# Performance work log

Hardware: AMD Instinct MI355X
Metric: run time of the kernel (lower is better)

## Reference

```python
import jax, jax.numpy as jnp
import numpy as np

N_NODES = 10000
N_EDGES = 160000
D_IN = 50
ALPHA = 0.2  # LeakyReLU negative slope


def _xavier(key, shape):
    fan_in, fan_out = shape[0], int(np.prod(shape[1:]))
    limit = float(np.sqrt(6.0 / (fan_in + fan_out)))
    return jax.random.uniform(key, shape, jnp.float32, -limit, limit)


def setup_inputs() -> dict:
    key = jax.random.key(0)
    ks = jax.random.split(key, 8)
    x = jax.random.normal(ks[0], (N_NODES, D_IN), jnp.float32)
    edge_idx = jax.random.randint(ks[1], (2, N_EDGES), 0, N_NODES, jnp.int64)
    # layer 1: 50 -> 4 heads x 256, concat
    W1 = _xavier(ks[2], (D_IN, 4, 256))
    a1 = _xavier(ks[3], (4, 512))  # [H, 2F]: split into a_src, a_dst
    # layer 2: 1024 -> 4 heads x 256, concat
    W2 = _xavier(ks[4], (1024, 4, 256))
    a2 = _xavier(ks[5], (4, 512))
    # layer 3: 1024 -> 6 heads x 121, mean
    W3 = _xavier(ks[6], (1024, 6, 121))
    a3 = _xavier(ks[7], (6, 242))
    return {"x": x, "edge_idx": edge_idx, "W1": W1, "a1": a1,
            "W2": W2, "a2": a2, "W3": W3, "a3": a3}


def gat_layer(h, W, a, src, dst, aggregate):
    """Multi-head GAT layer over an edge list. h:[N,Din], W:[Din,H,F], a:[H,2F]."""
    N = h.shape[0]
    Wh = jnp.einsum('nd,dhf->nhf', h, W)                    # [N, H, F]
    F = Wh.shape[-1]
    att_src = jnp.einsum('nhf,hf->nh', Wh, a[:, :F])         # a^T [Wh_i || .]
    att_dst = jnp.einsum('nhf,hf->nh', Wh, a[:, F:])         # a^T [. || Wh_j]
    logits = jax.nn.leaky_relu(att_src[src] + att_dst[dst], ALPHA)  # [E, H]
    # numerically stable softmax over incoming edges of each destination node
    m = jax.ops.segment_max(logits, dst, num_segments=N)
    e = jnp.exp(logits - m[dst])
    denom = jax.ops.segment_sum(e, dst, num_segments=N)
    coef = e / (denom[dst] + 1e-16)                           # [E, H]
    out = jax.ops.segment_sum(coef[:, :, None] * Wh[src], dst, num_segments=N)
    if aggregate == 'concat':
        return out.reshape(N, -1)
    return out.mean(axis=1)


def reference(x, edge_idx, W1, a1, W2, a2, W3, a3):
    src, dst = edge_idx[0], edge_idx[1]
    h1 = jax.nn.elu(gat_layer(x, W1, a1, src, dst, 'concat'))   # [N, 1024]
    h2 = jax.nn.elu(gat_layer(h1, W2, a2, src, dst, 'concat'))  # [N, 1024]
    h3_in = h1 + h2                                              # residual skip
    return gat_layer(h3_in, W3, a3, src, dst, 'mean')            # [N, 121]
```

## Files before the change

kernel.cpp:

```cpp
#include <hip/hip_runtime.h>
#include <hip/hip_bf16.h>
#include <math.h>

#define NN 10000
#define NE 160000

typedef __attribute__((ext_vector_type(8))) _Float16 f16x8;
typedef __attribute__((ext_vector_type(4))) _Float16 f16x4;
typedef __attribute__((ext_vector_type(4))) float f32x4;

static __device__ __forceinline__ void gload_lds16(const _Float16* g, _Float16* l) {
  __builtin_amdgcn_global_load_lds((const __attribute__((address_space(1))) char*)g,
                                   (__attribute__((address_space(3))) char*)l, 16, 0, 0);
}

__global__ __launch_bounds__(1024) void scan_kernel(const int* __restrict__ counts,
                                                    int* __restrict__ row_ptr,
                                                    int* __restrict__ cursor, int N) {
  __shared__ int sums[1024];
  int t = threadIdx.x;
  const int CH = (N + 1023) >> 10;
  int base = t * CH;
  int s = 0;
  for (int i = 0; i < CH; ++i) { int idx = base + i; if (idx < N) s += counts[idx]; }
  sums[t] = s;
  __syncthreads();
  for (int off = 1; off < 1024; off <<= 1) {
    int v = 0;
    if (t >= off) v = sums[t - off];
    __syncthreads();
    if (t >= off) sums[t] += v;
    __syncthreads();
  }
  int run = (t == 0) ? 0 : sums[t - 1];
  for (int i = 0; i < CH; ++i) {
    int idx = base + i;
    if (idx < N) { row_ptr[idx] = run; cursor[idx] = run; run += counts[idx]; }
  }
  if (t == 0) row_ptr[N] = sums[1023];
}

__global__ void scatter_kernel(const int* __restrict__ src, const int* __restrict__ dst,
                               int* __restrict__ cursor, int* __restrict__ ssrc, int E) {
  int e = blockIdx.x * blockDim.x + threadIdx.x;
  if (e < E) {
    int pos = atomicAdd(&cursor[dst[e]], 1);
    ssrc[pos] = src[e];
  }
}

#define TB_W2 256
#define TB_W3 192
#define TB_W1 16
#define TB_T (TB_W2 + TB_W3 + TB_W1)
#define TB_X ((NN * 64) / 256)
#define TB_E ((NE + 255) / 256)
__global__ __launch_bounds__(256) void prep2(const float* __restrict__ x,
                                             const float* __restrict__ W1,
                                             const float* __restrict__ W2,
                                             const float* __restrict__ W3,
                                             const int* __restrict__ dst,
                                             int* __restrict__ counts,
                                             _Float16* __restrict__ xh,
                                             _Float16* __restrict__ w1,
                                             _Float16* __restrict__ w2,
                                             _Float16* __restrict__ w3) {
  int b = blockIdx.x;
  int t = threadIdx.x;
  if (b < TB_T) {
    const float* S;
    _Float16* D;
    int K, Nsrc, KP, k0, n0;
    if (b < TB_W2) {
      S = W2; D = w2; K = 1024; Nsrc = 1024; KP = 1024;
      k0 = (b & 15) * 64; n0 = (b >> 4) * 64;
    } else if (b < TB_W2 + TB_W3) {
      int bb = b - TB_W2;
      S = W3; D = w3; K = 1024; Nsrc = 726; KP = 1024;
      k0 = (bb & 15) * 64; n0 = (bb >> 4) * 64;
    } else {
      int bb = b - TB_W2 - TB_W3;
      S = W1; D = w1; K = 50; Nsrc = 1024; KP = 64;
      k0 = 0; n0 = bb * 64;
    }
    __shared__ float tile[64][65];
#pragma unroll
    for (int i = 0; i < 16; ++i) {
      int idx = i * 256 + t;
      int r = idx >> 6, c = idx & 63;
      int gk = k0 + r, gn = n0 + c;
      tile[r][c] = (gk < K && gn < Nsrc) ? S[(size_t)gk * Nsrc + gn] : 0.f;
    }
    __syncthreads();
#pragma unroll
    for (int i = 0; i < 16; ++i) {
      int idx = i * 256 + t;
      int r = idx >> 6, c = idx & 63;
      D[(size_t)(n0 + r) * KP + k0 + c] = (_Float16)tile[c][r];
    }
    return;
  }
  int i = (b - TB_T) * 256 + t;
  if (i < NN * 64) {
    int m = i >> 6, k = i & 63;
    xh[i] = (_Float16)(k < 50 ? x[m * 50 + k] : 0.f);
    return;
  }
  i -= NN * 64;
  if (i < NE) atomicAdd(&counts[dst[i]], 1);
}

template<int PAD121>
__global__ __launch_bounds__(256) void gemm_f16(const _Float16* __restrict__ A,
                                                const _Float16* __restrict__ B,
                                                _Float16* __restrict__ C,
                                                int M, int KP, int NC) {
  int flat = blockIdx.x;
  int xcd = flat & 7;
  int slot = flat >> 3;
  int cblk = slot % NC;
  int rblk = (slot / NC) * 8 + xcd;
  const int m0 = rblk * 128;
  if (m0 >= M) return;
  const int n0 = cblk * 128;

  __shared__ _Float16 As[128 * 64];
  __shared__ _Float16 Bs[128 * 64];

  const int t = threadIdx.x;
  const int lane = t & 63;
  const int wid = t >> 6;
  const int wr = wid >> 1;
  const int wc = wid & 1;
  const int row_in = lane & 15;
  const int kgrp = lane >> 4;

  const int srow = wid * 32 + ((lane >> 3) & 7);
  const int sl7 = lane & 7;

  f32x4 acc[4][4];
#pragma unroll
  for (int i = 0; i < 4; ++i)
#pragma unroll
    for (int j = 0; j < 4; ++j) acc[i][j] = (f32x4){0.f, 0.f, 0.f, 0.f};

  for (int k0 = 0; k0 < KP; k0 += 64) {
    if (k0) __syncthreads();
#pragma unroll
    for (int j = 0; j < 4; ++j) {
      int row = srow + j * 8;
      int gs = (sl7 ^ (row & 7)) * 8;
      int gm = m0 + row;
      if (gm >= M) gm = M - 1;
      _Float16* ldsA = &As[(wid * 32 + j * 8) * 64];
      _Float16* ldsB = &Bs[(wid * 32 + j * 8) * 64];
      gload_lds16(&A[(size_t)gm * KP + k0 + gs], ldsA);
      gload_lds16(&B[(size_t)(n0 + row) * KP + k0 + gs], ldsB);
    }
    __syncthreads();

#pragma unroll
    for (int ks = 0; ks < 2; ++ks) {
      f16x8 a[4], b[4];
#pragma unroll
      for (int mi = 0; mi < 4; ++mi) {
        int arow = wr * 64 + mi * 16 + row_in;
        int ps = ((kgrp + ks * 4) ^ (arow & 7)) * 8;
        a[mi] = *(const f16x8*)&As[arow * 64 + ps];
      }
#pragma unroll
      for (int ni = 0; ni < 4; ++ni) {
        int brow = wc * 64 + ni * 16 + row_in;
        int ps = ((kgrp + ks * 4) ^ (brow & 7)) * 8;
        b[ni] = *(const f16x8*)&Bs[brow * 64 + ps];
      }
#pragma unroll
      for (int mi = 0; mi < 4; ++mi)
#pragma unroll
        for (int ni = 0; ni < 4; ++ni)
          acc[mi][ni] = __builtin_amdgcn_mfma_f32_16x16x32_f16(a[mi], b[ni], acc[mi][ni], 0, 0, 0);
    }
  }

#pragma unroll
  for (int mi = 0; mi < 4; ++mi) {
#pragma unroll
    for (int ni = 0; ni < 4; ++ni) {
      int gn = n0 + wc * 64 + ni * 16 + row_in;
#pragma unroll
      for (int j = 0; j < 4; ++j) {
        int gm = m0 + wr * 64 + mi * 16 + kgrp * 4 + j;
        if (gm >= M) continue;
        if (PAD121) {
          if (gn < 726) {
            int h = gn / 121;
            int pc = h * 128 + (gn - h * 121);
            C[(size_t)gm * 768 + pc] = (_Float16)acc[mi][ni][j];
          }
        } else {
          C[(size_t)gm * 1024 + gn] = (_Float16)acc[mi][ni][j];
        }
      }
    }
  }
}

template<int H, int F, int SW, int HS>
__global__ void att_kernel(const _Float16* __restrict__ Whb, const float* __restrict__ a,
                           float* __restrict__ att_s, float* __restrict__ att_d, int N) {
  int n = blockIdx.x;
  int h = threadIdx.x >> 6;
  int lane = threadIdx.x & 63;
  const _Float16* w = Whb + (size_t)n * SW + h * HS;
  const float* as = a + (size_t)h * 2 * F;
  const float* ad = as + F;
  float ss = 0.f, sd = 0.f;
  for (int f = lane; f < F; f += 64) {
    float v = (float)w[f];
    ss += v * as[f];
    sd += v * ad[f];
  }
#pragma unroll
  for (int off = 32; off > 0; off >>= 1) {
    ss += __shfl_down(ss, off);
    sd += __shfl_down(sd, off);
  }
  if (lane == 0) {
    att_s[n * H + h] = ss;
    att_d[n * H + h] = sd;
  }
}

template<int H>
__global__ __launch_bounds__(256) void edge_softmax_csr(const int* __restrict__ row_ptr,
                                                        const int* __restrict__ ssrc,
                                                        const float* __restrict__ att_s,
                                                        const float* __restrict__ att_d,
                                                        float* __restrict__ cbuf,
                                                        float* __restrict__ dinv, int N) {
  int n = blockIdx.x * 16 + (threadIdx.x >> 4);
  if (n >= N) return;
  int lane = threadIdx.x & 15;
  int beg = row_ptr[n], end = row_ptr[n + 1];

  float ad[H];
  if (H == 4) {
    f32x4 v = *(const f32x4*)&att_d[n * 4];
    ad[0] = v.x; ad[1] = v.y; ad[2] = v.z; ad[3] = v.w;
  } else {
#pragma unroll
    for (int h = 0; h < H; ++h) ad[h] = att_d[n * H + h];
  }

  float m[H];
#pragma unroll
  for (int h = 0; h < H; ++h) m[h] = -INFINITY;
  for (int k = beg + lane; k < end; k += 16) {
    int s = ssrc[k];
    float as[H];
    if (H == 4) {
      f32x4 v = *(const f32x4*)&att_s[s * 4];
      as[0] = v.x; as[1] = v.y; as[2] = v.z; as[3] = v.w;
    } else {
#pragma unroll
      for (int h = 0; h < H; ++h) as[h] = att_s[s * H + h];
    }
#pragma unroll
    for (int h = 0; h < H; ++h) {
      float xv = as[h] + ad[h];
      float l = xv >= 0.f ? xv : 0.2f * xv;
      m[h] = fmaxf(m[h], l);
    }
  }
#pragma unroll
  for (int h = 0; h < H; ++h)
#pragma unroll
    for (int off = 8; off > 0; off >>= 1) m[h] = fmaxf(m[h], __shfl_xor(m[h], off));

  float sum[H];
#pragma unroll
  for (int h = 0; h < H; ++h) sum[h] = 0.f;
  for (int k = beg + lane; k < end; k += 16) {
    int s = ssrc[k];
    float as[H];
    if (H == 4) {
      f32x4 v = *(const f32x4*)&att_s[s * 4];
      as[0] = v.x; as[1] = v.y; as[2] = v.z; as[3] = v.w;
    } else {
#pragma unroll
      for (int h = 0; h < H; ++h) as[h] = att_s[s * H + h];
    }
    float ev[H];
#pragma unroll
    for (int h = 0; h < H; ++h) {
      float xv = as[h] + ad[h];
      float l = xv >= 0.f ? xv : 0.2f * xv;
      ev[h] = __expf(l - m[h]);
      sum[h] += ev[h];
    }
    if (H == 4) {
      *(f32x4*)&cbuf[(size_t)k * 4] = (f32x4){ev[0], ev[1], ev[2], ev[3]};
    } else {
#pragma unroll
      for (int h = 0; h < H; ++h) cbuf[(size_t)k * H + h] = ev[h];
    }
  }
#pragma unroll
  for (int h = 0; h < H; ++h) {
#pragma unroll
    for (int off = 8; off > 0; off >>= 1) sum[h] += __shfl_xor(sum[h], off);
  }
  if (lane < H) dinv[n * H + lane] = 1.f / (sum[lane] + 1e-16f);
}

template<int MODE>
__global__ __launch_bounds__(256) void aggregate_cat_chunk(const int* __restrict__ row_ptr,
                                                           const int* __restrict__ ssrc,
                                                           const float* __restrict__ cbuf,
                                                           const float* __restrict__ dinv,
                                                           const _Float16* __restrict__ Whb,
                                                           const _Float16* __restrict__ h1,
                                                           _Float16* __restrict__ outv, int N) {
  int b = blockIdx.x;
  int chunk = b & 7;
  int group = b >> 3;
  int n = group * 16 + (threadIdx.x >> 4);
  if (n >= N) return;
  int tt = threadIdx.x & 15;
  int idx = chunk * 128 + tt * 8;
  int h = chunk >> 1;
  float inv = dinv[n * 4 + h];

  float acc[8] = {};
  int beg = row_ptr[n], end = row_ptr[n + 1];
  int k = beg;
  for (; k + 1 < end; k += 2) {
    int s0 = ssrc[k], s1 = ssrc[k + 1];
    float c0 = cbuf[(size_t)k * 4 + h];
    float c1 = cbuf[(size_t)(k + 1) * 4 + h];
    f16x8 w0 = *(const f16x8*)&Whb[(size_t)s0 * 1024 + idx];
    f16x8 w1 = *(const f16x8*)&Whb[(size_t)s1 * 1024 + idx];
#pragma unroll
    for (int j = 0; j < 8; ++j) {
      acc[j] += c0 * (float)w0[j];
      acc[j] += c1 * (float)w1[j];
    }
  }
  if (k < end) {
    int s0 = ssrc[k];
    float c0 = cbuf[(size_t)k * 4 + h];
    f16x8 w0 = *(const f16x8*)&Whb[(size_t)s0 * 1024 + idx];
#pragma unroll
    for (int j = 0; j < 8; ++j) acc[j] += c0 * (float)w0[j];
  }

  size_t o = (size_t)n * 1024 + idx;
  f16x8 r1;
  if (MODE == 1) r1 = *(const f16x8*)&h1[o];
  f16x8 vo;
#pragma unroll
  for (int j = 0; j < 8; ++j) {
    float v = acc[j] * inv;
    v = v > 0.f ? v : expm1f(v);
    if (MODE == 1) v += (float)r1[j];
    vo[j] = (_Float16)v;
  }
  *(f16x8*)&outv[o] = vo;
}

__global__ __launch_bounds__(256) void aggregate_mean_chunk(const int* __restrict__ row_ptr,
                                                            const int* __restrict__ ssrc,
                                                            const float* __restrict__ cbuf,
                                                            const float* __restrict__ dinv,
                                                            const _Float16* __restrict__ Whb,
                                                            float* __restrict__ part, int N) {
  int b = blockIdx.x;
  int h = b & 7;
  if (h >= 6) return;
  int n = (b >> 3) * 16 + (threadIdx.x >> 4);
  if (n >= N) return;
  int tt = threadIdx.x & 15;
  int base = h * 128 + tt * 8;
  float inv = dinv[n * 6 + h];

  float acc[8] = {};
  int beg = row_ptr[n], end = row_ptr[n + 1];
  int k = beg;
  for (; k + 1 < end; k += 2) {
    int s0 = ssrc[k], s1 = ssrc[k + 1];
    float c0 = cbuf[(size_t)k * 6 + h];
    float c1 = cbuf[(size_t)(k + 1) * 6 + h];
    f16x8 w0 = *(const f16x8*)&Whb[(size_t)s0 * 768 + base];
    f16x8 w1 = *(const f16x8*)&Whb[(size_t)s1 * 768 + base];
#pragma unroll
    for (int j = 0; j < 8; ++j) {
      acc[j] += c0 * (float)w0[j];
      acc[j] += c1 * (float)w1[j];
    }
  }
  if (k < end) {
    int s0 = ssrc[k];
    float c0 = cbuf[(size_t)k * 6 + h];
    f16x8 w0 = *(const f16x8*)&Whb[(size_t)s0 * 768 + base];
#pragma unroll
    for (int j = 0; j < 8; ++j) acc[j] += c0 * (float)w0[j];
  }

  float* p = &part[(size_t)n * 768 + base];
  *(f32x4*)&p[0] = (f32x4){acc[0] * inv, acc[1] * inv, acc[2] * inv, acc[3] * inv};
  *(f32x4*)&p[4] = (f32x4){acc[4] * inv, acc[5] * inv, acc[6] * inv, acc[7] * inv};
}

__global__ __launch_bounds__(128) void reduce_mean(const float* __restrict__ part,
                                                   float* __restrict__ out, int N) {
  int n = blockIdx.x;
  int f = threadIdx.x;
  if (f >= 121) return;
  const float* p = &part[(size_t)n * 768];
  float s = 0.f;
#pragma unroll
  for (int h = 0; h < 6; ++h) s += p[h * 128 + f];
  out[(size_t)n * 121 + f] = s * (1.0f / 6.0f);
}

extern "C" void kernel_launch(void* const* d_in, const int* in_sizes, int n_in,
                              void* d_out, int out_size, void* d_ws, size_t ws_size,
                              hipStream_t stream) {
  const float* x  = (const float*)d_in[0];
  const int* eidx = (const int*)d_in[1];
  const float* W1 = (const float*)d_in[2];
  const float* a1 = (const float*)d_in[3];
  const float* W2 = (const float*)d_in[4];
  const float* a2 = (const float*)d_in[5];
  const float* W3 = (const float*)d_in[6];
  const float* a3 = (const float*)d_in[7];
  float* out = (float*)d_out;

  const int N = NN, E = NE;
  const int* src = eidx;
  const int* dst = eidx + E;

  char* ws = (char*)d_ws;
  size_t off = 0;
  auto alloc = [&](size_t bytes) -> void* {
    void* p = ws + off;
    off += (bytes + 255) & ~(size_t)255;
    return p;
  };
  _Float16* Whf  = (_Float16*)alloc((size_t)N * 1024 * 2);
  _Float16* h1   = (_Float16*)alloc((size_t)N * 1024 * 2);
  _Float16* hsum = (_Float16*)alloc((size_t)N * 1024 * 2);
  _Float16* xh   = (_Float16*)alloc((size_t)N * 64 * 2);
  _Float16* w1   = (_Float16*)alloc((size_t)1024 * 64 * 2);
  _Float16* w2   = (_Float16*)alloc((size_t)1024 * 1024 * 2);
  _Float16* w3   = (_Float16*)alloc((size_t)768 * 1024 * 2);
  float* cbuf  = (float*)alloc((size_t)E * 6 * 4);
  float* part  = (float*)alloc((size_t)N * 768 * 4);
  float* atts  = (float*)alloc((size_t)N * 6 * 4);
  float* attd  = (float*)alloc((size_t)N * 6 * 4);
  float* dinv  = (float*)alloc((size_t)N * 6 * 4);
  int* counts  = (int*)alloc((size_t)N * 4);
  int* row_ptr = (int*)alloc((size_t)(N + 1) * 4);
  int* cursor  = (int*)alloc((size_t)N * 4);
  int* ssrc    = (int*)alloc((size_t)E * 4);

  hipMemsetAsync(counts, 0, (size_t)N * 4, stream);
  prep2<<<TB_T + TB_X + TB_E, 256, 0, stream>>>(x, W1, W2, W3, dst, counts, xh, w1, w2, w3);
  scan_kernel<<<1, 1024, 0, stream>>>(counts, row_ptr, cursor, N);
  scatter_kernel<<<(E + 255) / 256, 256, 0, stream>>>(src, dst, cursor, ssrc, E);

  const int RPG = 10;
  const int AGG_GRID = 8 * ((N + 15) / 16);
  const int SM_GRID = (N + 15) / 16;

  gemm_f16<0><<<8 * RPG * 8, 256, 0, stream>>>(xh, w1, Whf, N, 64, 8);
  att_kernel<4, 256, 1024, 256><<<N, 256, 0, stream>>>(Whf, a1, atts, attd, N);
  edge_softmax_csr<4><<<SM_GRID, 256, 0, stream>>>(row_ptr, ssrc, atts, attd, cbuf, dinv, N);
  aggregate_cat_chunk<0><<<AGG_GRID, 256, 0, stream>>>(row_ptr, ssrc, cbuf, dinv, Whf, nullptr, h1, N);

  gemm_f16<0><<<8 * RPG * 8, 256, 0, stream>>>(h1, w2, Whf, N, 1024, 8);
  att_kernel<4, 256, 1024, 256><<<N, 256, 0, stream>>>(Whf, a2, atts, attd, N);
  edge_softmax_csr<4><<<SM_GRID, 256, 0, stream>>>(row_ptr, ssrc, atts, attd, cbuf, dinv, N);
  aggregate_cat_chunk<1><<<AGG_GRID, 256, 0, stream>>>(row_ptr, ssrc, cbuf, dinv, Whf, h1, hsum, N);

  gemm_f16<1><<<8 * RPG * 6, 256, 0, stream>>>(hsum, w3, Whf, N, 1024, 6);
  att_kernel<6, 121, 768, 128><<<N, 384, 0, stream>>>(Whf, a3, atts, attd, N);
  edge_softmax_csr<6><<<SM_GRID, 256, 0, stream>>>(row_ptr, ssrc, atts, attd, cbuf, dinv, N);
  aggregate_mean_chunk<<<AGG_GRID, 256, 0, stream>>>(row_ptr, ssrc, cbuf, dinv, Whf, part, N);
  reduce_mean<<<N, 128, 0, stream>>>(part, out, N);
}
```

Before: 276.7 us.

## Fuse edge softmax into aggregation kernels, recomputing coefficients per chunk

```diff
diff --git a/kernel.cpp b/kernel.cpp
--- a/kernel.cpp
+++ b/kernel.cpp
@@ -231,96 +231,14 @@
   }
 }
 
-template<int H>
-__global__ __launch_bounds__(256) void edge_softmax_csr(const int* __restrict__ row_ptr,
-                                                        const int* __restrict__ ssrc,
-                                                        const float* __restrict__ att_s,
-                                                        const float* __restrict__ att_d,
-                                                        float* __restrict__ cbuf,
-                                                        float* __restrict__ dinv, int N) {
-  int n = blockIdx.x * 16 + (threadIdx.x >> 4);
-  if (n >= N) return;
-  int lane = threadIdx.x & 15;
-  int beg = row_ptr[n], end = row_ptr[n + 1];
-
-  float ad[H];
-  if (H == 4) {
-    f32x4 v = *(const f32x4*)&att_d[n * 4];
-    ad[0] = v.x; ad[1] = v.y; ad[2] = v.z; ad[3] = v.w;
-  } else {
-#pragma unroll
-    for (int h = 0; h < H; ++h) ad[h] = att_d[n * H + h];
-  }
-
-  float m[H];
-#pragma unroll
-  for (int h = 0; h < H; ++h) m[h] = -INFINITY;
-  for (int k = beg + lane; k < end; k += 16) {
-    int s = ssrc[k];
-    float as[H];
-    if (H == 4) {
-      f32x4 v = *(const f32x4*)&att_s[s * 4];
-      as[0] = v.x; as[1] = v.y; as[2] = v.z; as[3] = v.w;
-    } else {
-#pragma unroll
-      for (int h = 0; h < H; ++h) as[h] = att_s[s * H + h];
-    }
-#pragma unroll
-    for (int h = 0; h < H; ++h) {
-      float xv = as[h] + ad[h];
-      float l = xv >= 0.f ? xv : 0.2f * xv;
-      m[h] = fmaxf(m[h], l);
-    }
-  }
-#pragma unroll
-  for (int h = 0; h < H; ++h)
-#pragma unroll
-    for (int off = 8; off > 0; off >>= 1) m[h] = fmaxf(m[h], __shfl_xor(m[h], off));
-
-  float sum[H];
-#pragma unroll
-  for (int h = 0; h < H; ++h) sum[h] = 0.f;
-  for (int k = beg + lane; k < end; k += 16) {
-    int s = ssrc[k];
-    float as[H];
-    if (H == 4) {
-      f32x4 v = *(const f32x4*)&att_s[s * 4];
-      as[0] = v.x; as[1] = v.y; as[2] = v.z; as[3] = v.w;
-    } else {
-#pragma unroll
-      for (int h = 0; h < H; ++h) as[h] = att_s[s * H + h];
-    }
-    float ev[H];
-#pragma unroll
-    for (int h = 0; h < H; ++h) {
-      float xv = as[h] + ad[h];
-      float l = xv >= 0.f ? xv : 0.2f * xv;
-      ev[h] = __expf(l - m[h]);
-      sum[h] += ev[h];
-    }
-    if (H == 4) {
-      *(f32x4*)&cbuf[(size_t)k * 4] = (f32x4){ev[0], ev[1], ev[2], ev[3]};
-    } else {
-#pragma unroll
-      for (int h = 0; h < H; ++h) cbuf[(size_t)k * H + h] = ev[h];
-    }
-  }
-#pragma unroll
-  for (int h = 0; h < H; ++h) {
-#pragma unroll
-    for (int off = 8; off > 0; off >>= 1) sum[h] += __shfl_xor(sum[h], off);
-  }
-  if (lane < H) dinv[n * H + lane] = 1.f / (sum[lane] + 1e-16f);
-}
-
 template<int MODE>
-__global__ __launch_bounds__(256) void aggregate_cat_chunk(const int* __restrict__ row_ptr,
-                                                           const int* __restrict__ ssrc,
-                                                           const float* __restrict__ cbuf,
-                                                           const float* __restrict__ dinv,
-                                                           const _Float16* __restrict__ Whb,
-                                                           const _Float16* __restrict__ h1,
-                                                           _Float16* __restrict__ outv, int N) {
+__global__ __launch_bounds__(256) void agg_cat_fused(const int* __restrict__ row_ptr,
+                                                     const int* __restrict__ ssrc,
+                                                     const float* __restrict__ atts,
+                                                     const float* __restrict__ attd,
+                                                     const _Float16* __restrict__ Whb,
+                                                     const _Float16* __restrict__ h1,
+                                                     _Float16* __restrict__ outv, int N) {
   int b = blockIdx.x;
   int chunk = b & 7;
   int group = b >> 3;
@@ -329,15 +247,37 @@
   int tt = threadIdx.x & 15;
   int idx = chunk * 128 + tt * 8;
   int h = chunk >> 1;
-  float inv = dinv[n * 4 + h];
+  int beg = row_ptr[n], end = row_ptr[n + 1];
+  float adh = attd[n * 4 + h];
+
+  float m = -1e30f;
+  for (int k = beg + tt; k < end; k += 16) {
+    float xv = atts[ssrc[k] * 4 + h] + adh;
+    float l = xv >= 0.f ? xv : 0.2f * xv;
+    m = fmaxf(m, l);
+  }
+#pragma unroll
+  for (int off = 8; off > 0; off >>= 1) m = fmaxf(m, __shfl_xor(m, off));
+  float s = 0.f;
+  for (int k = beg + tt; k < end; k += 16) {
+    float xv = atts[ssrc[k] * 4 + h] + adh;
+    float l = xv >= 0.f ? xv : 0.2f * xv;
+    s += __expf(l - m);
+  }
+#pragma unroll
+  for (int off = 8; off > 0; off >>= 1) s += __shfl_xor(s, off);
+  float inv = 1.f / (s + 1e-16f);
 
   float acc[8] = {};
-  int beg = row_ptr[n], end = row_ptr[n + 1];
   int k = beg;
   for (; k + 1 < end; k += 2) {
     int s0 = ssrc[k], s1 = ssrc[k + 1];
-    float c0 = cbuf[(size_t)k * 4 + h];
-    float c1 = cbuf[(size_t)(k + 1) * 4 + h];
+    float x0 = atts[s0 * 4 + h] + adh;
+    float x1 = atts[s1 * 4 + h] + adh;
+    x0 = x0 >= 0.f ? x0 : 0.2f * x0;
+    x1 = x1 >= 0.f ? x1 : 0.2f * x1;
+    float c0 = __expf(x0 - m) * inv;
+    float c1 = __expf(x1 - m) * inv;
     f16x8 w0 = *(const f16x8*)&Whb[(size_t)s0 * 1024 + idx];
     f16x8 w1 = *(const f16x8*)&Whb[(size_t)s1 * 1024 + idx];
 #pragma unroll
@@ -348,7 +288,9 @@
   }
   if (k < end) {
     int s0 = ssrc[k];
-    float c0 = cbuf[(size_t)k * 4 + h];
+    float x0 = atts[s0 * 4 + h] + adh;
+    x0 = x0 >= 0.f ? x0 : 0.2f * x0;
+    float c0 = __expf(x0 - m) * inv;
     f16x8 w0 = *(const f16x8*)&Whb[(size_t)s0 * 1024 + idx];
 #pragma unroll
     for (int j = 0; j < 8; ++j) acc[j] += c0 * (float)w0[j];
@@ -360,7 +302,7 @@
   f16x8 vo;
 #pragma unroll
   for (int j = 0; j < 8; ++j) {
-    float v = acc[j] * inv;
+    float v = acc[j];
     v = v > 0.f ? v : expm1f(v);
     if (MODE == 1) v += (float)r1[j];
     vo[j] = (_Float16)v;
@@ -368,12 +310,12 @@
   *(f16x8*)&outv[o] = vo;
 }
 
-__global__ __launch_bounds__(256) void aggregate_mean_chunk(const int* __restrict__ row_ptr,
-                                                            const int* __restrict__ ssrc,
-                                                            const float* __restrict__ cbuf,
-                                                            const float* __restrict__ dinv,
-                                                            const _Float16* __restrict__ Whb,
-                                                            float* __restrict__ part, int N) {
+__global__ __launch_bounds__(256) void agg_mean_fused(const int* __restrict__ row_ptr,
+                                                      const int* __restrict__ ssrc,
+                                                      const float* __restrict__ atts,
+                                                      const float* __restrict__ attd,
+                                                      const _Float16* __restrict__ Whb,
+                                                      float* __restrict__ part, int N) {
   int b = blockIdx.x;
   int h = b & 7;
   if (h >= 6) return;
@@ -381,15 +323,37 @@
   if (n >= N) return;
   int tt = threadIdx.x & 15;
   int base = h * 128 + tt * 8;
-  float inv = dinv[n * 6 + h];
+  int beg = row_ptr[n], end = row_ptr[n + 1];
+  float adh = attd[n * 6 + h];
+
+  float m = -1e30f;
+  for (int k = beg + tt; k < end; k += 16) {
+    float xv = atts[ssrc[k] * 6 + h] + adh;
+    float l = xv >= 0.f ? xv : 0.2f * xv;
+    m = fmaxf(m, l);
+  }
+#pragma unroll
+  for (int off = 8; off > 0; off >>= 1) m = fmaxf(m, __shfl_xor(m, off));
+  float s = 0.f;
+  for (int k = beg + tt; k < end; k += 16) {
+    float xv = atts[ssrc[k] * 6 + h] + adh;
+    float l = xv >= 0.f ? xv : 0.2f * xv;
+    s += __expf(l - m);
+  }
+#pragma unroll
+  for (int off = 8; off > 0; off >>= 1) s += __shfl_xor(s, off);
+  float inv = 1.f / (s + 1e-16f);
 
   float acc[8] = {};
-  int beg = row_ptr[n], end = row_ptr[n + 1];
   int k = beg;
   for (; k + 1 < end; k += 2) {
     int s0 = ssrc[k], s1 = ssrc[k + 1];
-    float c0 = cbuf[(size_t)k * 6 + h];
-    float c1 = cbuf[(size_t)(k + 1) * 6 + h];
+    float x0 = atts[s0 * 6 + h] + adh;
+    float x1 = atts[s1 * 6 + h] + adh;
+    x0 = x0 >= 0.f ? x0 : 0.2f * x0;
+    x1 = x1 >= 0.f ? x1 : 0.2f * x1;
+    float c0 = __expf(x0 - m) * inv;
+    float c1 = __expf(x1 - m) * inv;
     f16x8 w0 = *(const f16x8*)&Whb[(size_t)s0 * 768 + base];
     f16x8 w1 = *(const f16x8*)&Whb[(size_t)s1 * 768 + base];
 #pragma unroll
@@ -400,15 +364,17 @@
   }
   if (k < end) {
     int s0 = ssrc[k];
-    float c0 = cbuf[(size_t)k * 6 + h];
+    float x0 = atts[s0 * 6 + h] + adh;
+    x0 = x0 >= 0.f ? x0 : 0.2f * x0;
+    float c0 = __expf(x0 - m) * inv;
     f16x8 w0 = *(const f16x8*)&Whb[(size_t)s0 * 768 + base];
 #pragma unroll
     for (int j = 0; j < 8; ++j) acc[j] += c0 * (float)w0[j];
   }
 
   float* p = &part[(size_t)n * 768 + base];
-  *(f32x4*)&p[0] = (f32x4){acc[0] * inv, acc[1] * inv, acc[2] * inv, acc[3] * inv};
-  *(f32x4*)&p[4] = (f32x4){acc[4] * inv, acc[5] * inv, acc[6] * inv, acc[7] * inv};
+  *(f32x4*)&p[0] = (f32x4){acc[0], acc[1], acc[2], acc[3]};
+  *(f32x4*)&p[4] = (f32x4){acc[4], acc[5], acc[6], acc[7]};
 }
 
 __global__ __launch_bounds__(128) void reduce_mean(const float* __restrict__ part,
@@ -454,11 +420,9 @@
   _Float16* w1   = (_Float16*)alloc((size_t)1024 * 64 * 2);
   _Float16* w2   = (_Float16*)alloc((size_t)1024 * 1024 * 2);
   _Float16* w3   = (_Float16*)alloc((size_t)768 * 1024 * 2);
-  float* cbuf  = (float*)alloc((size_t)E * 6 * 4);
   float* part  = (float*)alloc((size_t)N * 768 * 4);
   float* atts  = (float*)alloc((size_t)N * 6 * 4);
   float* attd  = (float*)alloc((size_t)N * 6 * 4);
-  float* dinv  = (float*)alloc((size_t)N * 6 * 4);
   int* counts  = (int*)alloc((size_t)N * 4);
   int* row_ptr = (int*)alloc((size_t)(N + 1) * 4);
   int* cursor  = (int*)alloc((size_t)N * 4);
@@ -471,21 +435,17 @@
 
   const int RPG = 10;
   const int AGG_GRID = 8 * ((N + 15) / 16);
-  const int SM_GRID = (N + 15) / 16;
 
   gemm_f16<0><<<8 * RPG * 8, 256, 0, stream>>>(xh, w1, Whf, N, 64, 8);
   att_kernel<4, 256, 1024, 256><<<N, 256, 0, stream>>>(Whf, a1, atts, attd, N);
-  edge_softmax_csr<4><<<SM_GRID, 256, 0, stream>>>(row_ptr, ssrc, atts, attd, cbuf, dinv, N);
-  aggregate_cat_chunk<0><<<AGG_GRID, 256, 0, stream>>>(row_ptr, ssrc, cbuf, dinv, Whf, nullptr, h1, N);
+  agg_cat_fused<0><<<AGG_GRID, 256, 0, stream>>>(row_ptr, ssrc, atts, attd, Whf, nullptr, h1, N);
 
   gemm_f16<0><<<8 * RPG * 8, 256, 0, stream>>>(h1, w2, Whf, N, 1024, 8);
   att_kernel<4, 256, 1024, 256><<<N, 256, 0, stream>>>(Whf, a2, atts, attd, N);
-  edge_softmax_csr<4><<<SM_GRID, 256, 0, stream>>>(row_ptr, ssrc, atts, attd, cbuf, dinv, N);
-  aggregate_cat_chunk<1><<<AGG_GRID, 256, 0, stream>>>(row_ptr, ssrc, cbuf, dinv, Whf, h1, hsum, N);
+  agg_cat_fused<1><<<AGG_GRID, 256, 0, stream>>>(row_ptr, ssrc, atts, attd, Whf, h1, hsum, N);
 
   gemm_f16<1><<<8 * RPG * 6, 256, 0, stream>>>(hsum, w3, Whf, N, 1024, 6);
   att_kernel<6, 121, 768, 128><<<N, 384, 0, stream>>>(Whf, a3, atts, attd, N);
-  edge_softmax_csr<6><<<SM_GRID, 256, 0, stream>>>(row_ptr, ssrc, atts, attd, cbuf, dinv, N);
-  aggregate_mean_chunk<<<AGG_GRID, 256, 0, stream>>>(row_ptr, ssrc, cbuf, dinv, Whf, part, N);
+  agg_mean_fused<<<AGG_GRID, 256, 0, stream>>>(row_ptr, ssrc, atts, attd, Whf, part, N);
   reduce_mean<<<N, 128, 0, stream>>>(part, out, N);
 }
```

Result: slower. 286.3 us (+3.5%).
